# Kernel tuning notes

Hardware: AMD Instinct MI355X
Metric: run time of the kernel (lower is better)

Reference implementation:

```python
import jax, jax.numpy as jnp
import numpy as np
import math

B, L, IN_DIM, OUT_DIM = 2, 2048, 128, 128
H, DH = 8, 32            # num_heads, dim_head
ED = H * DH * 2          # embed_dim = 512
DEPTH = 1
LAMBDA_INIT = 0.8 - 0.6 * math.exp(-0.3 * (DEPTH + 1))
EPS = 1e-8


def setup_inputs() -> dict:
    key = jax.random.key(0)
    ks = jax.random.split(key, 10)
    x = jax.random.normal(ks[0], (B, 1, L, IN_DIM), dtype=jnp.float32)
    mask_2d = jax.random.bernoulli(ks[1], 0.9, (B, L, L))
    Wq = jax.random.normal(ks[2], (IN_DIM, ED), dtype=jnp.float32) * 0.05
    Wkv = jax.random.normal(ks[3], (IN_DIM, 2 * ED), dtype=jnp.float32) * 0.05
    Wout = jax.random.normal(ks[4], (ED, OUT_DIM), dtype=jnp.float32) * 0.05
    lambda_q1 = jax.random.normal(ks[5], (DH,), dtype=jnp.float32) * 0.1
    lambda_k1 = jax.random.normal(ks[6], (DH,), dtype=jnp.float32) * 0.1
    lambda_q2 = jax.random.normal(ks[7], (DH,), dtype=jnp.float32) * 0.1
    lambda_k2 = jax.random.normal(ks[8], (DH,), dtype=jnp.float32) * 0.1
    gamma = jnp.ones((2 * DH,), dtype=jnp.float32)
    return {"x": x, "mask_2d": mask_2d, "Wq": Wq, "Wkv": Wkv, "Wout": Wout,
            "lambda_q1": lambda_q1, "lambda_k1": lambda_k1,
            "lambda_q2": lambda_q2, "lambda_k2": lambda_k2, "gamma": gamma}


def reference(x, mask_2d, Wq, Wkv, Wout, lambda_q1, lambda_k1, lambda_q2, lambda_k2, gamma):
    b = x.shape[0]
    xs = x[:, 0]                                   # [b, L, in_dim]
    q = xs @ Wq                                    # [b, L, 2*H*DH]
    k, v = jnp.split(xs @ Wkv, 2, axis=-1)
    q = q.reshape(b, L, 2 * H, DH).transpose(0, 2, 1, 3) * (DH ** -0.5)  # [b,2H,L,d]
    k = k.reshape(b, L, 2 * H, DH).transpose(0, 2, 1, 3)                 # [b,2H,L,d]
    v = v.reshape(b, L, H, 2 * DH).transpose(0, 2, 1, 3)                 # [b,H,L,2d]
    dots = jnp.einsum('bnld,bnmd->bnlm', q, k)     # [b,2H,L,L]
    mask_value = -jnp.finfo(dots.dtype).max
    dots = jnp.where(mask_2d[:, None, :, :], dots, mask_value)
    attn_w = jax.nn.softmax(dots.astype(jnp.float32), axis=-1).astype(dots.dtype)
    lam1 = jnp.exp(jnp.sum(lambda_q1 * lambda_k1))
    lam2 = jnp.exp(jnp.sum(lambda_q2 * lambda_k2))
    lam = lam1 - lam2 + LAMBDA_INIT
    attn_w = attn_w.reshape(b, H, 2, L, L)
    attn_w = attn_w[:, :, 0] - lam * attn_w[:, :, 1]   # [b,H,L,L]
    attn = jnp.einsum('bhlm,bhmd->bhld', attn_w, v)    # [b,H,L,2d]
    rms = jnp.sqrt(jnp.mean(attn ** 2, axis=-1, keepdims=True))
    attn = gamma * (attn / (rms + EPS)) * (1.0 - LAMBDA_INIT)
    out = attn.transpose(0, 2, 1, 3).reshape(b, L, H * 2 * DH) @ Wout  # [b,L,out_dim]
    return out[:, None]                             # [b,1,L,out_dim]
```

## Files before the change

kernel.cpp:

```cpp
#include <hip/hip_runtime.h>
#include <float.h>
#include <math.h>

typedef __attribute__((ext_vector_type(8))) short short8;
typedef __attribute__((ext_vector_type(4))) float f32x4;
typedef __attribute__((ext_vector_type(4))) unsigned short ushort4v;

constexpr int SEQL = 2048;
constexpr int NQH  = 16;
constexpr int NVH  = 8;
constexpr int DHD  = 32;
constexpr float LAMB_INIT = 0.4707130183436648f;
constexpr float REPS      = 1e-8f;
constexpr float QW        = 0.25503492f;

#if __has_builtin(__builtin_amdgcn_exp2f)
#define EXPW(x) __builtin_amdgcn_exp2f(x)
#else
#define EXPW(x) exp2f(x)
#endif

static __device__ __forceinline__ unsigned short f2bf(float f) {
    union { float f; unsigned u; } a; a.f = f;
    unsigned u = a.u;
    u += 0x7fffu + ((u >> 16) & 1u);
    return (unsigned short)(u >> 16);
}

static __device__ __forceinline__ unsigned cvtpk(float lo, float hi) {
    unsigned r;
    asm("v_cvt_pk_bf16_f32 %0, %1, %2" : "=v"(r) : "v"(lo), "v"(hi));
    return r;
}

static __device__ __forceinline__ void stage16(const unsigned short* g, unsigned short* l) {
    __builtin_amdgcn_global_load_lds(
        (const __attribute__((address_space(1))) unsigned int*)g,
        (__attribute__((address_space(3))) unsigned int*)l, 16, 0, 0);
}

__global__ __launch_bounds__(256) void pack_prep_kernel(
        const unsigned char* __restrict__ mb, const int* __restrict__ mi,
        unsigned long long* __restrict__ bits,
        const float* __restrict__ x, const float* __restrict__ Wq,
        const float* __restrict__ Wkv, const float* __restrict__ Wout,
        unsigned short* __restrict__ xb, unsigned short* __restrict__ Wf,
        unsigned short* __restrict__ WfO) {
    __shared__ int cnt[256];
    int t = threadIdx.x;
    int c = 0;
    #pragma unroll
    for (int i = 0; i < 16; ++i) c += (mb[t * 16 + i] != 0);
    cnt[t] = c;
    __syncthreads();
    for (int s = 128; s > 0; s >>= 1) { if (t < s) cnt[t] += cnt[t + s]; __syncthreads(); }
    int f = cnt[0] > 2048;
    int gtid = blockIdx.x * 256 + t;
    int nthr = gridDim.x * 256;
    {
        const int total = 2 * SEQL * (SEQL / 64);
        int wid = blockIdx.x * 4 + (t >> 6);
        int lane = t & 63;
        int stride = gridDim.x * 4;
        for (int w = wid; w < total; w += stride) {
            int e = w * 64 + lane;
            int v = f ? (int)mb[e] : mi[e];
            unsigned long long b = __ballot(v != 0);
            if (lane == 0) bits[w] = b;
        }
    }
    {
        float4 v = ((const float4*)x)[gtid];
        ushort4v o = { f2bf(v.x), f2bf(v.y), f2bf(v.z), f2bf(v.w) };
        ((ushort4v*)xb)[gtid] = o;
    }
    for (int e = gtid; e < 262144; e += nthr) {
        int k = e >> 11, cc = e & 2047;
        if (cc < 1536) {
            float v = (cc < 512) ? Wq[(size_t)k * 512 + cc] * QW
                                 : Wkv[(size_t)k * 1024 + (cc - 512)];
            int cp = cc >> 4, lr = cc & 15, kk = k >> 5, lg = (k >> 3) & 3, j = k & 7;
            Wf[(((size_t)(cp * 4 + kk) * 4 + lg) * 16 + lr) * 8 + j] = f2bf(v);
        }
    }
    if (gtid < 65536) {
        int k = gtid >> 7, cc = gtid & 127;
        float v = Wout[gtid];
        int cp = cc >> 4, lr = cc & 15, kk = k >> 5, lg = (k >> 3) & 3, j = k & 7;
        WfO[(((size_t)(cp * 16 + kk) * 4 + lg) * 16 + lr) * 8 + j] = f2bf(v);
    }
}

__global__ __launch_bounds__(256) void qkv_mfma_kernel(
        const unsigned short* __restrict__ xb, const unsigned short* __restrict__ Wf,
        unsigned short* __restrict__ Q, unsigned short* __restrict__ Kf,
        unsigned short* __restrict__ Vf) {
    int t = threadIdx.x, w = t >> 6, lane = t & 63, lr = lane & 15, lg = lane >> 4;
    int lid = blockIdx.x;
    int swz = (lid & 7) * 192 + (lid >> 3);
    int by = swz >> 6, bx = swz & 63;
    int r0 = bx * 64 + w * 16;
    short8 ax[4];
    #pragma unroll
    for (int kk = 0; kk < 4; ++kk)
        ax[kk] = *(const short8*)(xb + (size_t)(r0 + lr) * 128 + kk * 32 + lg * 8);
    f32x4 acc[4];
    #pragma unroll
    for (int ct = 0; ct < 4; ++ct) acc[ct] = (f32x4){0.f, 0.f, 0.f, 0.f};
    #pragma unroll
    for (int ct = 0; ct < 4; ++ct) {
        int cp = by * 4 + ct;
        #pragma unroll
        for (int kk = 0; kk < 4; ++kk) {
            short8 bw = *(const short8*)(Wf + (size_t)(cp * 4 + kk) * 512 + lane * 8);
            acc[ct] = __builtin_amdgcn_mfma_f32_16x16x32_bf16(ax[kk], bw, acc[ct], 0, 0, 0);
        }
    }
    int gr0 = r0 + 4 * lg;
    int b = gr0 >> 11;
    if (by < 8) {
        #pragma unroll
        for (int ct = 0; ct < 4; ++ct) {
            int col = by * 64 + 16 * ct + lr;
            int n = col >> 5, d = col & 31;
            #pragma unroll
            for (int r = 0; r < 4; ++r) {
                int l = (gr0 + r) & 2047;
                Q[(((size_t)(b * NQH + n)) * SEQL + l) * DHD + d] = f2bf(acc[ct][r]);
            }
        }
    } else if (by < 16) {
        #pragma unroll
        for (int ct = 0; ct < 4; ++ct) {
            int ck = by * 64 + 16 * ct + lr - 512;
            int n = ck >> 5, dk = ck & 31;
            size_t hb = ((size_t)(b * NQH + n)) * 65536 + (dk >> 3) * 128 + (dk & 7);
            #pragma unroll
            for (int r = 0; r < 4; ++r) {
                int l = (gr0 + r) & 2047;
                Kf[hb + (size_t)((l >> 6) * 4 + ((l >> 4) & 3)) * 512 + (l & 15) * 8]
                    = f2bf(acc[ct][r]);
            }
        }
    } else {
        #pragma unroll
        for (int ct = 0; ct < 4; ++ct) {
            int cv = by * 64 + 16 * ct + lr - 1024;
            int h = cv >> 6, d = cv & 63;
            size_t hb = ((size_t)(b * NVH + h)) * 131072 + (d >> 4) * 512 + (d & 15) * 8;
            #pragma unroll
            for (int r = 0; r < 4; ++r) {
                int l = (gr0 + r) & 2047;
                Vf[hb + (size_t)((l >> 6) * 2 + ((l >> 5) & 1)) * 2048
                      + ((l >> 4) & 1) * 4 + ((l >> 2) & 3) * 128 + (l & 3)]
                    = f2bf(acc[ct][r]);
            }
        }
    }
}

__global__ __launch_bounds__(256, 2) void attn_kernel(
        const unsigned short* __restrict__ Q, const unsigned short* __restrict__ Kf,
        const unsigned short* __restrict__ Vf, const unsigned long long* __restrict__ bits,
        const float* __restrict__ lq1, const float* __restrict__ lk1,
        const float* __restrict__ lq2, const float* __restrict__ lk2,
        const float* __restrict__ gamma, unsigned short* __restrict__ A) {
    __shared__ unsigned short lds[4][8192];
    int tid = threadIdx.x;
    int w = tid >> 6, lane = tid & 63;
    int lr = lane & 15, lg = lane >> 4;
    int lid = blockIdx.y * 32 + blockIdx.x;
    int swz = (lid & 7) * 64 + (lid >> 3);
    int qtile = swz & 31, bh = swz >> 5;
    int b = bh >> 3, h = bh & 7;
    int q0 = qtile * 64 + w * 16;
    int bnA = b * NQH + 2 * h;

    short8 aqA = *(const short8*)(Q + (((size_t)bnA) * SEQL + q0 + lr) * DHD + lg * 8);
    short8 aqB = *(const short8*)(Q + (((size_t)(bnA + 1)) * SEQL + q0 + lr) * DHD + lg * 8);
    const unsigned short* KA = Kf + ((size_t)bnA) * 65536;
    const unsigned short* KB = KA + 65536;
    const unsigned short* VB = Vf + ((size_t)(b * NVH + h)) * 131072;
    const unsigned long long* mrow = bits + ((size_t)b * SEQL + q0 + lr) * 32;

    auto stage_tile = [&](int bf, int it) {
        #pragma unroll
        for (int j = 0; j < 4; ++j) {
            int c = 4 * w + j;
            const unsigned short* src =
                (c < 4) ? (KA + it * 2048 + c * 512)
              : (c < 8) ? (KB + it * 2048 + (c - 4) * 512)
                        : (VB + it * 4096 + (c - 8) * 512);
            stage16(src + lane * 8, &lds[bf][c * 512]);
        }
    };

    f32x4 oA[4], oB[4];
    #pragma unroll
    for (int m = 0; m < 4; ++m) { oA[m] = (f32x4){0,0,0,0}; oB[m] = (f32x4){0,0,0,0}; }
    float ssA = 0.f, ssB = 0.f;
    unsigned long long mw = mrow[0];

    short8 paE[4], paO[4], bvE[8], bvO[8];
    #pragma unroll
    for (int i = 0; i < 4; ++i) { paE[i] = (short8){0,0,0,0,0,0,0,0}; paO[i] = (short8){0,0,0,0,0,0,0,0}; }
    #pragma unroll
    for (int i = 0; i < 8; ++i) { bvE[i] = (short8){0,0,0,0,0,0,0,0}; bvO[i] = (short8){0,0,0,0,0,0,0,0}; }

    stage_tile(0, 0);
    stage_tile(1, 1);

    auto body = [&](int t, short8* pa, short8* pbv, short8* npa, short8* nbv) {
        unsigned long long mwc = mw;
        mw = mrow[(t + 1) & 31];
        stage_tile((t + 2) & 3, (t + 2) & 31);
        asm volatile("s_waitcnt vmcnt(10)" ::: "memory");
        __builtin_amdgcn_s_barrier();
        __builtin_amdgcn_sched_barrier(0);
        const unsigned short* L = &lds[t & 3][0];
        short8 bkA[4], bkB[4];
        #pragma unroll
        for (int c = 0; c < 4; ++c) bkA[c] = *(const short8*)(L + c * 512 + lane * 8);
        #pragma unroll
        for (int c = 0; c < 4; ++c) bkB[c] = *(const short8*)(L + 2048 + c * 512 + lane * 8);
        #pragma unroll
        for (int z = 0; z < 8; ++z) nbv[z] = *(const short8*)(L + 4096 + z * 512 + lane * 8);
        f32x4 sA[4], sB[4];
        __builtin_amdgcn_s_setprio(1);
        #pragma unroll
        for (int c = 0; c < 4; ++c)
            sA[c] = __builtin_amdgcn_mfma_f32_16x16x32_bf16(bkA[c], aqA, (f32x4){0,0,0,0}, 0, 0, 0);
        #pragma unroll
        for (int c = 0; c < 4; ++c)
            sB[c] = __builtin_amdgcn_mfma_f32_16x16x32_bf16(bkB[c], aqB, (f32x4){0,0,0,0}, 0, 0, 0);
        #pragma unroll
        for (int m = 0; m < 4; ++m) {
            oA[m] = __builtin_amdgcn_mfma_f32_16x16x32_bf16(pa[0], pbv[m], oA[m], 0, 0, 0);
            oB[m] = __builtin_amdgcn_mfma_f32_16x16x32_bf16(pa[2], pbv[m], oB[m], 0, 0, 0);
        }
        #pragma unroll
        for (int m = 0; m < 4; ++m) {
            oA[m] = __builtin_amdgcn_mfma_f32_16x16x32_bf16(pa[1], pbv[4 + m], oA[m], 0, 0, 0);
            oB[m] = __builtin_amdgcn_mfma_f32_16x16x32_bf16(pa[3], pbv[4 + m], oB[m], 0, 0, 0);
        }
        __builtin_amdgcn_s_setprio(0);
        unsigned long long mwl = mwc >> (4 * lg);
        unsigned mlo = (unsigned)mwl, mhi = (unsigned)(mwl >> 32);
        float pA[4][4], pB[4][4];
        #pragma unroll
        for (int c = 0; c < 4; ++c) {
            unsigned wv = (c < 2) ? mlo : mhi;
            int sh = (c & 1) * 16;
            #pragma unroll
            for (int r = 0; r < 4; ++r) {
                unsigned keep = (wv >> (sh + r)) & 1u;
                float eA = EXPW(sA[c][r]);
                float eB = EXPW(sB[c][r]);
                pA[c][r] = keep ? eA : 0.f;
                pB[c][r] = keep ? eB : 0.f;
            }
        }
        float acA = 0.f, acB = 0.f;
        #pragma unroll
        for (int c = 0; c < 4; ++c)
            #pragma unroll
            for (int r = 0; r < 4; ++r) { acA += pA[c][r]; acB += pB[c][r]; }
        ssA += acA; ssB += acB;
        union { short8 v; unsigned u[4]; } a0, a1, b0, b1;
        a0.u[0] = cvtpk(pA[0][0], pA[0][1]); a0.u[1] = cvtpk(pA[0][2], pA[0][3]);
        a0.u[2] = cvtpk(pA[1][0], pA[1][1]); a0.u[3] = cvtpk(pA[1][2], pA[1][3]);
        a1.u[0] = cvtpk(pA[2][0], pA[2][1]); a1.u[1] = cvtpk(pA[2][2], pA[2][3]);
        a1.u[2] = cvtpk(pA[3][0], pA[3][1]); a1.u[3] = cvtpk(pA[3][2], pA[3][3]);
        b0.u[0] = cvtpk(pB[0][0], pB[0][1]); b0.u[1] = cvtpk(pB[0][2], pB[0][3]);
        b0.u[2] = cvtpk(pB[1][0], pB[1][1]); b0.u[3] = cvtpk(pB[1][2], pB[1][3]);
        b1.u[0] = cvtpk(pB[2][0], pB[2][1]); b1.u[1] = cvtpk(pB[2][2], pB[2][3]);
        b1.u[2] = cvtpk(pB[3][0], pB[3][1]); b1.u[3] = cvtpk(pB[3][2], pB[3][3]);
        npa[0] = a0.v; npa[1] = a1.v; npa[2] = b0.v; npa[3] = b1.v;
    };

    for (int tp = 0; tp < 16; ++tp) {
        body(2 * tp,     paE, bvE, paO, bvO);
        body(2 * tp + 1, paO, bvO, paE, bvE);
    }
    #pragma unroll
    for (int m = 0; m < 4; ++m) {
        oA[m] = __builtin_amdgcn_mfma_f32_16x16x32_bf16(paE[0], bvE[m], oA[m], 0, 0, 0);
        oB[m] = __builtin_amdgcn_mfma_f32_16x16x32_bf16(paE[2], bvE[m], oB[m], 0, 0, 0);
    }
    #pragma unroll
    for (int m = 0; m < 4; ++m) {
        oA[m] = __builtin_amdgcn_mfma_f32_16x16x32_bf16(paE[1], bvE[4 + m], oA[m], 0, 0, 0);
        oB[m] = __builtin_amdgcn_mfma_f32_16x16x32_bf16(paE[3], bvE[4 + m], oB[m], 0, 0, 0);
    }
    ssA += __shfl_xor(ssA, 16, 64); ssA += __shfl_xor(ssA, 32, 64);
    ssB += __shfl_xor(ssB, 16, 64); ssB += __shfl_xor(ssB, 32, 64);
    float invA = 1.f / ssA, invB = 1.f / ssB;
    float iA[4], iB[4];
    #pragma unroll
    for (int r = 0; r < 4; ++r) {
        iA[r] = __shfl(invA, 4 * lg + r, 64);
        iB[r] = __shfl(invB, 4 * lg + r, 64);
    }
    int l31 = lane & 31;
    float t1 = lq1[l31] * lk1[l31];
    float t2 = lq2[l31] * lk2[l31];
    #pragma unroll
    for (int o = 1; o < 32; o <<= 1) { t1 += __shfl_xor(t1, o, 64); t2 += __shfl_xor(t2, o, 64); }
    float lam = __expf(t1) - __expf(t2) + LAMB_INIT;
    float dv[4][4];
    float sq[4] = {0.f, 0.f, 0.f, 0.f};
    #pragma unroll
    for (int m = 0; m < 4; ++m)
        #pragma unroll
        for (int r = 0; r < 4; ++r) {
            float v = oA[m][r] * iA[r] - lam * (oB[m][r] * iB[r]);
            dv[m][r] = v;
            sq[r] += v * v;
        }
    #pragma unroll
    for (int r = 0; r < 4; ++r) {
        #pragma unroll
        for (int o = 1; o < 16; o <<= 1) sq[r] += __shfl_xor(sq[r], o, 64);
        sq[r] = (1.f - LAMB_INIT) / (sqrtf(sq[r] * (1.f / 64.f)) + REPS);
    }
    float gm[4];
    #pragma unroll
    for (int m = 0; m < 4; ++m) gm[m] = gamma[16 * m + lr];
    unsigned short* Ab = A + ((size_t)(b * SEQL + q0 + 4 * lg)) * 512 + h * 64 + lr;
    #pragma unroll
    for (int m = 0; m < 4; ++m)
        #pragma unroll
        for (int r = 0; r < 4; ++r)
            Ab[(size_t)r * 512 + 16 * m] = f2bf(dv[m][r] * sq[r] * gm[m]);
}

__global__ __launch_bounds__(64) void proj_mfma_kernel(
        const unsigned short* __restrict__ Ab, const unsigned short* __restrict__ WfO,
        float* __restrict__ out) {
    int lane = threadIdx.x & 63, lr = lane & 15, lg = lane >> 4;
    int r0 = blockIdx.x * 16;
    f32x4 acc[8];
    #pragma unroll
    for (int ct = 0; ct < 8; ++ct) acc[ct] = (f32x4){0.f, 0.f, 0.f, 0.f};
    #pragma unroll
    for (int kk = 0; kk < 16; ++kk) {
        short8 af = *(const short8*)(Ab + (size_t)(r0 + lr) * 512 + kk * 32 + lg * 8);
        #pragma unroll
        for (int ct = 0; ct < 8; ++ct) {
            short8 bf = *(const short8*)(WfO + (size_t)(ct * 16 + kk) * 512 + lane * 8);
            acc[ct] = __builtin_amdgcn_mfma_f32_16x16x32_bf16(af, bf, acc[ct], 0, 0, 0);
        }
    }
    #pragma unroll
    for (int ct = 0; ct < 8; ++ct)
        #pragma unroll
        for (int r = 0; r < 4; ++r)
            out[(size_t)(r0 + 4 * lg + r) * 128 + ct * 16 + lr] = acc[ct][r];
}

extern "C" void kernel_launch(void* const* d_in, const int* in_sizes, int n_in,
                              void* d_out, int out_size, void* d_ws, size_t ws_size,
                              hipStream_t stream) {
    const float* x    = (const float*)d_in[0];
    const void*  mask = d_in[1];
    const float* Wq   = (const float*)d_in[2];
    const float* Wkv  = (const float*)d_in[3];
    const float* Wout = (const float*)d_in[4];
    const float* lq1  = (const float*)d_in[5];
    const float* lk1  = (const float*)d_in[6];
    const float* lq2  = (const float*)d_in[7];
    const float* lk2  = (const float*)d_in[8];
    const float* gam  = (const float*)d_in[9];
    float* out = (float*)d_out;

    char* wsb = (char*)d_ws;
    unsigned long long* bits = (unsigned long long*)(wsb + 4096);
    unsigned short* Q        = (unsigned short*)(wsb + 1052672);
    unsigned short* Kf       = (unsigned short*)(wsb + 5246976);
    unsigned short* Vf       = (unsigned short*)(wsb + 9441280);
    unsigned short* xb       = (unsigned short*)(wsb + 13635584);
    unsigned short* Wf       = (unsigned short*)(wsb + 14684160);
    unsigned short* WfO      = (unsigned short*)(wsb + 15077376);
    unsigned short* Ab       = (unsigned short*)(wsb + 15208448);

    pack_prep_kernel<<<512, 256, 0, stream>>>((const unsigned char*)mask,
                                              (const int*)mask, bits,
                                              x, Wq, Wkv, Wout, xb, Wf, WfO);
    qkv_mfma_kernel<<<1536, 256, 0, stream>>>(xb, Wf, Q, Kf, Vf);
    attn_kernel<<<dim3(32, 16), 256, 0, stream>>>(Q, Kf, Vf, bits,
                                                  lq1, lk1, lq2, lk2, gam, Ab);
    proj_mfma_kernel<<<256, 64, 0, stream>>>(Ab, WfO, out);
}
```

Measured before the change: 93.89 us.

## Fuse mask packing and x conversion into QKV kernel, split-K projection

Moves mask bit-packing and the fp32-to-bf16 conversion of x out of the prep kernel and into the QKV MFMA kernel, which now reads x directly and converts it with packed cvt instructions. The prep kernel becomes a slimmer weight-only repack with a smaller grid. The output projection switches from one wave per block to four waves doing split-K, with an LDS reduction. Attention now uses an inline v_exp_f32 and adds an explicit vmcnt wait. Together these are meant to cut the extra xb round trip through memory and raise occupancy in projection, at the cost of a heavier QKV kernel and redundant mask-count work in every block.

```diff
diff --git a/kernel.cpp b/kernel.cpp
--- a/kernel.cpp
+++ b/kernel.cpp
@@ -4,7 +4,6 @@
 
 typedef __attribute__((ext_vector_type(8))) short short8;
 typedef __attribute__((ext_vector_type(4))) float f32x4;
-typedef __attribute__((ext_vector_type(4))) unsigned short ushort4v;
 
 constexpr int SEQL = 2048;
 constexpr int NQH  = 16;
@@ -14,12 +13,6 @@
 constexpr float REPS      = 1e-8f;
 constexpr float QW        = 0.25503492f;
 
-#if __has_builtin(__builtin_amdgcn_exp2f)
-#define EXPW(x) __builtin_amdgcn_exp2f(x)
-#else
-#define EXPW(x) exp2f(x)
-#endif
-
 static __device__ __forceinline__ unsigned short f2bf(float f) {
     union { float f; unsigned u; } a; a.f = f;
     unsigned u = a.u;
@@ -33,48 +26,26 @@
     return r;
 }
 
+static __device__ __forceinline__ float expv(float x) {
+    float r;
+    asm("v_exp_f32 %0, %1" : "=v"(r) : "v"(x));
+    return r;
+}
+
 static __device__ __forceinline__ void stage16(const unsigned short* g, unsigned short* l) {
     __builtin_amdgcn_global_load_lds(
         (const __attribute__((address_space(1))) unsigned int*)g,
         (__attribute__((address_space(3))) unsigned int*)l, 16, 0, 0);
 }
 
-__global__ __launch_bounds__(256) void pack_prep_kernel(
-        const unsigned char* __restrict__ mb, const int* __restrict__ mi,
-        unsigned long long* __restrict__ bits,
-        const float* __restrict__ x, const float* __restrict__ Wq,
-        const float* __restrict__ Wkv, const float* __restrict__ Wout,
-        unsigned short* __restrict__ xb, unsigned short* __restrict__ Wf,
-        unsigned short* __restrict__ WfO) {
-    __shared__ int cnt[256];
-    int t = threadIdx.x;
-    int c = 0;
-    #pragma unroll
-    for (int i = 0; i < 16; ++i) c += (mb[t * 16 + i] != 0);
-    cnt[t] = c;
-    __syncthreads();
-    for (int s = 128; s > 0; s >>= 1) { if (t < s) cnt[t] += cnt[t + s]; __syncthreads(); }
-    int f = cnt[0] > 2048;
-    int gtid = blockIdx.x * 256 + t;
-    int nthr = gridDim.x * 256;
-    {
-        const int total = 2 * SEQL * (SEQL / 64);
-        int wid = blockIdx.x * 4 + (t >> 6);
-        int lane = t & 63;
-        int stride = gridDim.x * 4;
-        for (int w = wid; w < total; w += stride) {
-            int e = w * 64 + lane;
-            int v = f ? (int)mb[e] : mi[e];
-            unsigned long long b = __ballot(v != 0);
-            if (lane == 0) bits[w] = b;
-        }
-    }
-    {
-        float4 v = ((const float4*)x)[gtid];
-        ushort4v o = { f2bf(v.x), f2bf(v.y), f2bf(v.z), f2bf(v.w) };
-        ((ushort4v*)xb)[gtid] = o;
-    }
-    for (int e = gtid; e < 262144; e += nthr) {
+__global__ __launch_bounds__(256) void wprep_kernel(
+        const float* __restrict__ Wq, const float* __restrict__ Wkv,
+        const float* __restrict__ Wout,
+        unsigned short* __restrict__ Wf, unsigned short* __restrict__ WfO) {
+    int gtid = blockIdx.x * 256 + threadIdx.x;
+    #pragma unroll
+    for (int i = 0; i < 4; ++i) {
+        int e = gtid + i * 65536;
         int k = e >> 11, cc = e & 2047;
         if (cc < 1536) {
             float v = (cc < 512) ? Wq[(size_t)k * 512 + cc] * QW
@@ -83,7 +54,7 @@
             Wf[(((size_t)(cp * 4 + kk) * 4 + lg) * 16 + lr) * 8 + j] = f2bf(v);
         }
     }
-    if (gtid < 65536) {
+    {
         int k = gtid >> 7, cc = gtid & 127;
         float v = Wout[gtid];
         int cp = cc >> 4, lr = cc & 15, kk = k >> 5, lg = (k >> 3) & 3, j = k & 7;
@@ -91,19 +62,40 @@
     }
 }
 
-__global__ __launch_bounds__(256) void qkv_mfma_kernel(
-        const unsigned short* __restrict__ xb, const unsigned short* __restrict__ Wf,
+__global__ __launch_bounds__(256) void qkv_mask_kernel(
+        const float* __restrict__ x, const unsigned short* __restrict__ Wf,
+        const unsigned char* __restrict__ mb, const int* __restrict__ mi,
+        unsigned long long* __restrict__ bits,
         unsigned short* __restrict__ Q, unsigned short* __restrict__ Kf,
         unsigned short* __restrict__ Vf) {
+    __shared__ int cnt[256];
     int t = threadIdx.x, w = t >> 6, lane = t & 63, lr = lane & 15, lg = lane >> 4;
+    {
+        int c = 0;
+        #pragma unroll
+        for (int i = 0; i < 16; ++i) c += (mb[t * 16 + i] != 0);
+        cnt[t] = c;
+    }
+    __syncthreads();
+    for (int s = 128; s > 0; s >>= 1) { if (t < s) cnt[t] += cnt[t + s]; __syncthreads(); }
+    int f = cnt[0] > 2048;
     int lid = blockIdx.x;
     int swz = (lid & 7) * 192 + (lid >> 3);
     int by = swz >> 6, bx = swz & 63;
     int r0 = bx * 64 + w * 16;
     short8 ax[4];
     #pragma unroll
-    for (int kk = 0; kk < 4; ++kk)
-        ax[kk] = *(const short8*)(xb + (size_t)(r0 + lr) * 128 + kk * 32 + lg * 8);
+    for (int kk = 0; kk < 4; ++kk) {
+        const float* xp = x + (size_t)(r0 + lr) * 128 + kk * 32 + lg * 8;
+        float4 v0 = *(const float4*)xp;
+        float4 v1 = *(const float4*)(xp + 4);
+        union { short8 v; unsigned u[4]; } ua;
+        ua.u[0] = cvtpk(v0.x, v0.y);
+        ua.u[1] = cvtpk(v0.z, v0.w);
+        ua.u[2] = cvtpk(v1.x, v1.y);
+        ua.u[3] = cvtpk(v1.z, v1.w);
+        ax[kk] = ua.v;
+    }
     f32x4 acc[4];
     #pragma unroll
     for (int ct = 0; ct < 4; ++ct) acc[ct] = (f32x4){0.f, 0.f, 0.f, 0.f};
@@ -156,6 +148,13 @@
                     = f2bf(acc[ct][r]);
             }
         }
+    }
+    int wd0 = blockIdx.x * 4 + w;
+    for (int wd = wd0; wd < 131072; wd += 6144) {
+        int e = wd * 64 + lane;
+        int v = f ? (int)mb[e] : mi[e];
+        unsigned long long bl = __ballot(v != 0);
+        if (lane == 0) bits[wd] = bl;
     }
 }
 
@@ -188,9 +187,9 @@
         for (int j = 0; j < 4; ++j) {
             int c = 4 * w + j;
             const unsigned short* src =
-                (c < 4) ? (KA + it * 2048 + c * 512)
-              : (c < 8) ? (KB + it * 2048 + (c - 4) * 512)
-                        : (VB + it * 4096 + (c - 8) * 512);
+                (c < 4) ? (KA + (size_t)it * 2048 + c * 512)
+              : (c < 8) ? (KB + (size_t)it * 2048 + (c - 4) * 512)
+                        : (VB + (size_t)it * 4096 + (c - 8) * 512);
             stage16(src + lane * 8, &lds[bf][c * 512]);
         }
     };
@@ -254,8 +253,8 @@
             #pragma unroll
             for (int r = 0; r < 4; ++r) {
                 unsigned keep = (wv >> (sh + r)) & 1u;
-                float eA = EXPW(sA[c][r]);
-                float eB = EXPW(sB[c][r]);
+                float eA = expv(sA[c][r]);
+                float eB = expv(sB[c][r]);
                 pA[c][r] = keep ? eA : 0.f;
                 pB[c][r] = keep ? eB : 0.f;
             }
@@ -292,6 +291,7 @@
         oA[m] = __builtin_amdgcn_mfma_f32_16x16x32_bf16(paE[1], bvE[4 + m], oA[m], 0, 0, 0);
         oB[m] = __builtin_amdgcn_mfma_f32_16x16x32_bf16(paE[3], bvE[4 + m], oB[m], 0, 0, 0);
     }
+    asm volatile("s_waitcnt vmcnt(0)" ::: "memory");
     ssA += __shfl_xor(ssA, 16, 64); ssA += __shfl_xor(ssA, 32, 64);
     ssB += __shfl_xor(ssB, 16, 64); ssB += __shfl_xor(ssB, 32, 64);
     float invA = 1.f / ssA, invB = 1.f / ssB;
@@ -334,16 +334,18 @@
             Ab[(size_t)r * 512 + 16 * m] = f2bf(dv[m][r] * sq[r] * gm[m]);
 }
 
-__global__ __launch_bounds__(64) void proj_mfma_kernel(
+__global__ __launch_bounds__(256) void proj_mfma_kernel(
         const unsigned short* __restrict__ Ab, const unsigned short* __restrict__ WfO,
         float* __restrict__ out) {
-    int lane = threadIdx.x & 63, lr = lane & 15, lg = lane >> 4;
+    __shared__ f32x4 red[1536];
+    int t = threadIdx.x, w = t >> 6, lane = t & 63, lr = lane & 15, lg = lane >> 4;
     int r0 = blockIdx.x * 16;
     f32x4 acc[8];
     #pragma unroll
     for (int ct = 0; ct < 8; ++ct) acc[ct] = (f32x4){0.f, 0.f, 0.f, 0.f};
     #pragma unroll
-    for (int kk = 0; kk < 16; ++kk) {
+    for (int j = 0; j < 4; ++j) {
+        int kk = w * 4 + j;
         short8 af = *(const short8*)(Ab + (size_t)(r0 + lr) * 512 + kk * 32 + lg * 8);
         #pragma unroll
         for (int ct = 0; ct < 8; ++ct) {
@@ -351,11 +353,25 @@
             acc[ct] = __builtin_amdgcn_mfma_f32_16x16x32_bf16(af, bf, acc[ct], 0, 0, 0);
         }
     }
-    #pragma unroll
-    for (int ct = 0; ct < 8; ++ct)
+    if (w) {
+        #pragma unroll
+        for (int ct = 0; ct < 8; ++ct)
+            red[((w - 1) * 8 + ct) * 64 + lane] = acc[ct];
+    }
+    __syncthreads();
+    if (w) return;
+    #pragma unroll
+    for (int ct = 0; ct < 8; ++ct) {
+        #pragma unroll
+        for (int j = 0; j < 3; ++j) {
+            f32x4 pv = red[(j * 8 + ct) * 64 + lane];
+            acc[ct][0] += pv[0]; acc[ct][1] += pv[1];
+            acc[ct][2] += pv[2]; acc[ct][3] += pv[3];
+        }
         #pragma unroll
         for (int r = 0; r < 4; ++r)
             out[(size_t)(r0 + 4 * lg + r) * 128 + ct * 16 + lr] = acc[ct][r];
+    }
 }
 
 extern "C" void kernel_launch(void* const* d_in, const int* in_sizes, int n_in,
@@ -378,16 +394,15 @@
     unsigned short* Q        = (unsigned short*)(wsb + 1052672);
     unsigned short* Kf       = (unsigned short*)(wsb + 5246976);
     unsigned short* Vf       = (unsigned short*)(wsb + 9441280);
-    unsigned short* xb       = (unsigned short*)(wsb + 13635584);
     unsigned short* Wf       = (unsigned short*)(wsb + 14684160);
     unsigned short* WfO      = (unsigned short*)(wsb + 15077376);
     unsigned short* Ab       = (unsigned short*)(wsb + 15208448);
 
-    pack_prep_kernel<<<512, 256, 0, stream>>>((const unsigned char*)mask,
-                                              (const int*)mask, bits,
-                                              x, Wq, Wkv, Wout, xb, Wf, WfO);
-    qkv_mfma_kernel<<<1536, 256, 0, stream>>>(xb, Wf, Q, Kf, Vf);
+    wprep_kernel<<<256, 256, 0, stream>>>(Wq, Wkv, Wout, Wf, WfO);
+    qkv_mask_kernel<<<1536, 256, 0, stream>>>(x, Wf,
+                                              (const unsigned char*)mask,
+                                              (const int*)mask, bits, Q, Kf, Vf);
     attn_kernel<<<dim3(32, 16), 256, 0, stream>>>(Q, Kf, Vf, bits,
                                                   lq1, lk1, lq2, lk2, gam, Ab);
-    proj_mfma_kernel<<<256, 64, 0, stream>>>(Ab, WfO, out);
-}
+    proj_mfma_kernel<<<256, 256, 0, stream>>>(Ab, WfO, out);
+}
```

New measurement: 90.99 us. 3.1% less time.
